# Performance work log

Measured on AMD Instinct MI355X. Metric: run time of the kernel, lower is better.

The kernel has to match this reference:

```python
import jax, jax.numpy as jnp
import numpy as np

N, D, K = 65536, 4096, 16
LN_EPS = 1e-5
SN_EPS = 1e-12
MIN_NORM = 1e-15


def setup_inputs() -> dict:
    key = jax.random.key(0)
    k1, k2, k3, k4 = jax.random.split(key, 4)
    return {
        "x": jax.random.normal(k1, (N, D), dtype=jnp.float32),
        "gamma": jnp.ones((D,), dtype=jnp.float32),
        "beta": jnp.zeros((D,), dtype=jnp.float32),
        "W": jax.random.normal(k2, (K, D), dtype=jnp.float32) * 0.02,
        "u": jax.random.normal(k3, (K,), dtype=jnp.float32),
        "log_scale": jnp.float32(-2.0),
    }


def _l2_normalize(v, eps=SN_EPS):
    return v / (jnp.linalg.norm(v) + eps)


def reference(x, gamma, beta, W, u, log_scale):
    # LayerNorm over last dim
    mean = jnp.mean(x, axis=-1, keepdims=True)
    var = jnp.mean(jnp.square(x - mean), axis=-1, keepdims=True)
    xn = (x - mean) * jax.lax.rsqrt(var + LN_EPS) * gamma + beta

    # spectral norm of W: one power iteration (torch spectral_norm forward)
    v = _l2_normalize(W.T @ u)           # [D]
    u_new = _l2_normalize(W @ v)         # [K]
    sigma = u_new @ (W @ v)              # scalar, top singular value estimate
    W_sn = W / sigma

    # linear (no bias) + learned scale
    vout = xn @ W_sn.T                   # [N, K]
    scale = jax.nn.sigmoid(log_scale) * 0.5
    vout = vout * scale

    # Poincare ball expmap0 with c=1: tanh(||v||) * v / ||v||
    vnorm = jnp.maximum(jnp.linalg.norm(vout, axis=-1, keepdims=True), MIN_NORM)
    return jnp.tanh(vnorm) * vout / vnorm
```

## Files before the change

### kernel.cpp

```cpp
#include <hip/hip_runtime.h>
#include <hip/hip_bf16.h>


#define ND 4096
#define NK 16
#define NROWS 65536

using f32x4  = __attribute__((ext_vector_type(4))) float;
using bf16x8 = __attribute__((ext_vector_type(8))) short;

#define GWB_OFF  0u
#define PART_OFF 131072u

__device__ __forceinline__ unsigned short f2bf(float f) {
    union { __hip_bfloat16 h; unsigned short u; } cv;
    cv.h = __float2bfloat16(f);
    return cv.u;
}

__global__ __launch_bounds__(256) void prep(
    const float* __restrict__ W, const float* __restrict__ gamma,
    const float* __restrict__ beta, const float* __restrict__ u,
    unsigned short* __restrict__ ws_gwb, float* __restrict__ ws_part)
{
    const int tid = threadIdx.x;
    const int d = blockIdx.x * 256 + tid;
    const int lane = tid & 63, wid = tid >> 6;

    float uu[NK];
#pragma unroll
    for (int k = 0; k < NK; ++k) uu[k] = u[k];
    const float g = gamma[d], b = beta[d];
    float w[NK];
#pragma unroll
    for (int k = 0; k < NK; ++k) w[k] = W[k * ND + d];

    float t = 0.f;
#pragma unroll
    for (int k = 0; k < NK; ++k) t = fmaf(w[k], uu[k], t);

    const int s  = d >> 5;
    const int wq = d & 31;
    const int lc = (wq >> 2) & 3;
    const int j  = (wq & 3) | ((wq >> 4) << 2);
    const int base = s * 512 + lc * 128 + j;

    float P[49];
#pragma unroll
    for (int k = 0; k < NK; ++k) {
        const float gw = g * w[k];
        ws_gwb[base + k * 8] = f2bf(gw);
        P[k]      = gw;
        P[16 + k] = b * w[k];
        P[32 + k] = w[k] * t;
    }
    P[48] = t * t;

#pragma unroll
    for (int m = 1; m < 64; m <<= 1) {
#pragma unroll
        for (int v = 0; v < 49; ++v) P[v] += __shfl_xor(P[v], m);
    }
    __shared__ float wred[4][49];
    if (lane == 0) {
#pragma unroll
        for (int v = 0; v < 49; ++v) wred[wid][v] = P[v];
    }
    __syncthreads();
    if (tid < 49)
        ws_part[blockIdx.x * 49 + tid] =
            (wred[0][tid] + wred[1][tid]) + (wred[2][tid] + wred[3][tid]);
}

__global__ __launch_bounds__(1024, 4) void hyp_main(
    const float* __restrict__ x, const unsigned short* __restrict__ gwb_g,
    const float* __restrict__ ws_part, const float* __restrict__ log_scale,
    float* __restrict__ out)
{
    __shared__ unsigned short gwb[ND * NK];
    __shared__ float scl[49];

    const int tid  = threadIdx.x;
    const int lane = tid & 63;
    const int wid  = tid >> 6;
    const int tile = (blockIdx.x << 4) + wid;
    const int lr = lane & 15;
    const int lc = lane >> 4;

    const float* xp = x + (size_t)(tile * 16 + lr) * ND + lc * 4;
    const unsigned short* lp = gwb + lane * 8;
    const int start = (tile * 53) & 63;

    const f32x4 xa0 = *(const f32x4*)(xp + start * 64);
    const f32x4 xb0 = *(const f32x4*)(xp + start * 64 + 16);
    const f32x4 xc0 = *(const f32x4*)(xp + start * 64 + 32);
    const f32x4 xd0 = *(const f32x4*)(xp + start * 64 + 48);

    {
        const uint4* src = (const uint4*)gwb_g;
        uint4* dst = (uint4*)gwb;
#pragma unroll
        for (int i = 0; i < 8; ++i)
            dst[tid + i * 1024] = src[tid + i * 1024];
    }
    if (tid < 49) {
        float s = 0.f;
#pragma unroll
        for (int b = 0; b < 16; ++b) s += ws_part[b * 49 + tid];
        scl[tid] = s;
    }
    __syncthreads();

    float ns2 = 0.f;
#pragma unroll
    for (int k = 0; k < NK; ++k) ns2 += scl[32 + k] * scl[32 + k];
    const float nt   = sqrtf(scl[48]) + 1e-12f;
    const float nwv  = sqrtf(ns2) / nt;
    const float sigma = (nwv * nwv) / (nwv + 1e-12f);
    const float coef = (0.5f / (1.0f + expf(-log_scale[0]))) / sigma;
    const float gk = scl[lr];
    const float bk = scl[16 + lr];

    f32x4 acc = {0.f, 0.f, 0.f, 0.f};
    float s1 = 0.f, s2 = 0.f;

#define HALF(XA, XB, SS) do {                                             \
        bf16x8 afrag;                                                     \
        afrag[0] = (short)f2bf(XA[0]); afrag[1] = (short)f2bf(XA[1]);     \
        afrag[2] = (short)f2bf(XA[2]); afrag[3] = (short)f2bf(XA[3]);     \
        afrag[4] = (short)f2bf(XB[0]); afrag[5] = (short)f2bf(XB[1]);     \
        afrag[6] = (short)f2bf(XB[2]); afrag[7] = (short)f2bf(XB[3]);     \
        s1 += ((XA[0] + XA[1]) + (XA[2] + XA[3]))                         \
            + ((XB[0] + XB[1]) + (XB[2] + XB[3]));                        \
        s2 = fmaf(XA[0], XA[0], s2); s2 = fmaf(XA[1], XA[1], s2);         \
        s2 = fmaf(XA[2], XA[2], s2); s2 = fmaf(XA[3], XA[3], s2);         \
        s2 = fmaf(XB[0], XB[0], s2); s2 = fmaf(XB[1], XB[1], s2);         \
        s2 = fmaf(XB[2], XB[2], s2); s2 = fmaf(XB[3], XB[3], s2);         \
        bf16x8 bfrag = *(const bf16x8*)(lp + (SS) * 512);                 \
        acc = __builtin_amdgcn_mfma_f32_16x16x32_bf16(afrag, bfrag, acc, 0, 0, 0); \
    } while (0)

#define PROCESS(II, XA, XB, XC, XD) do {                                  \
        HALF(XA, XB, 2 * (II));                                           \
        HALF(XC, XD, 2 * (II) + 1);                                       \
    } while (0)

#define LOADPROC(II) do {                                                 \
        f32x4 xa = *(const f32x4*)(xp + (II) * 64);                       \
        f32x4 xb = *(const f32x4*)(xp + (II) * 64 + 16);                  \
        f32x4 xc = *(const f32x4*)(xp + (II) * 64 + 32);                  \
        f32x4 xd = *(const f32x4*)(xp + (II) * 64 + 48);                  \
        PROCESS(II, xa, xb, xc, xd);                                      \
    } while (0)

    PROCESS(start, xa0, xb0, xc0, xd0);
#pragma unroll 2
    for (int i = start + 1; i < 64; ++i) LOADPROC(i);
#pragma unroll 2
    for (int i = 0; i < start; ++i) LOADPROC(i);
#undef LOADPROC
#undef PROCESS
#undef HALF

    s1 += __shfl_xor(s1, 16); s1 += __shfl_xor(s1, 32);
    s2 += __shfl_xor(s2, 16); s2 += __shfl_xor(s2, 32);
    const float mean = s1 * (1.0f / ND);
    const float var  = s2 * (1.0f / ND) - mean * mean;
    const float rstd = rsqrtf(var + 1e-5f);

    float vout[4];
#pragma unroll
    for (int j = 0; j < 4; ++j) {
        const int r = lc * 4 + j;
        const float m_r  = __shfl(mean, r);
        const float rs_r = __shfl(rstd, r);
        vout[j] = coef * (fmaf(-m_r, gk, acc[j]) * rs_r + bk);
    }

    float nsq[4];
#pragma unroll
    for (int j = 0; j < 4; ++j) nsq[j] = vout[j] * vout[j];
#pragma unroll
    for (int m = 1; m < 16; m <<= 1) {
#pragma unroll
        for (int j = 0; j < 4; ++j) nsq[j] += __shfl_xor(nsq[j], m);
    }

#pragma unroll
    for (int j = 0; j < 4; ++j) {
        float nv = sqrtf(nsq[j]);
        nv = fmaxf(nv, 1e-15f);
        const float fac = tanhf(nv) / nv;
        out[(size_t)(tile * 16 + lc * 4 + j) * NK + lr] = vout[j] * fac;
    }
}

extern "C" void kernel_launch(void* const* d_in, const int* in_sizes, int n_in,
                              void* d_out, int out_size, void* d_ws, size_t ws_size,
                              hipStream_t stream) {
    const float* x     = (const float*)d_in[0];
    const float* gamma = (const float*)d_in[1];
    const float* beta  = (const float*)d_in[2];
    const float* W     = (const float*)d_in[3];
    const float* u     = (const float*)d_in[4];
    const float* ls    = (const float*)d_in[5];

    char* ws = (char*)d_ws;
    unsigned short* ws_gwb = (unsigned short*)(ws + GWB_OFF);
    float* ws_part = (float*)(ws + PART_OFF);
    float* out     = (float*)d_out;

    prep<<<16, 256, 0, stream>>>(W, gamma, beta, u, ws_gwb, ws_part);
    hyp_main<<<256, 1024, 0, stream>>>(x, ws_gwb, ws_part, ls, out);
}
```

Measured before the change: 199.7 us.

## Fuse prep and main kernels into one cooperative launch with grid sync

Merges the small weight-prep kernel into the main kernel. The first 16 blocks compute the bf16 gamma*W table and the partial reductions, then every block waits on a cooperative grid-wide barrier before copying the table into LDS. The goal is to remove the second kernel launch and the gap between kernels, and to overlap the initial x prefetch with prep. In exchange it adds the cost of a grid barrier and requires all 256 blocks of 1024 threads to be co-resident, which the cooperative launch will reject if they are not.

```diff
diff --git a/kernel.cpp b/kernel.cpp
--- a/kernel.cpp
+++ b/kernel.cpp
@@ -1,5 +1,8 @@
 #include <hip/hip_runtime.h>
 #include <hip/hip_bf16.h>
+#include <hip/hip_cooperative_groups.h>
+
+namespace cg = cooperative_groups;
 
 
 #define ND 4096
@@ -18,66 +21,15 @@
     return cv.u;
 }
 
-__global__ __launch_bounds__(256) void prep(
-    const float* __restrict__ W, const float* __restrict__ gamma,
-    const float* __restrict__ beta, const float* __restrict__ u,
-    unsigned short* __restrict__ ws_gwb, float* __restrict__ ws_part)
-{
-    const int tid = threadIdx.x;
-    const int d = blockIdx.x * 256 + tid;
-    const int lane = tid & 63, wid = tid >> 6;
-
-    float uu[NK];
-#pragma unroll
-    for (int k = 0; k < NK; ++k) uu[k] = u[k];
-    const float g = gamma[d], b = beta[d];
-    float w[NK];
-#pragma unroll
-    for (int k = 0; k < NK; ++k) w[k] = W[k * ND + d];
-
-    float t = 0.f;
-#pragma unroll
-    for (int k = 0; k < NK; ++k) t = fmaf(w[k], uu[k], t);
-
-    const int s  = d >> 5;
-    const int wq = d & 31;
-    const int lc = (wq >> 2) & 3;
-    const int j  = (wq & 3) | ((wq >> 4) << 2);
-    const int base = s * 512 + lc * 128 + j;
-
-    float P[49];
-#pragma unroll
-    for (int k = 0; k < NK; ++k) {
-        const float gw = g * w[k];
-        ws_gwb[base + k * 8] = f2bf(gw);
-        P[k]      = gw;
-        P[16 + k] = b * w[k];
-        P[32 + k] = w[k] * t;
-    }
-    P[48] = t * t;
-
-#pragma unroll
-    for (int m = 1; m < 64; m <<= 1) {
-#pragma unroll
-        for (int v = 0; v < 49; ++v) P[v] += __shfl_xor(P[v], m);
-    }
-    __shared__ float wred[4][49];
-    if (lane == 0) {
-#pragma unroll
-        for (int v = 0; v < 49; ++v) wred[wid][v] = P[v];
-    }
-    __syncthreads();
-    if (tid < 49)
-        ws_part[blockIdx.x * 49 + tid] =
-            (wred[0][tid] + wred[1][tid]) + (wred[2][tid] + wred[3][tid]);
-}
-
-__global__ __launch_bounds__(1024, 4) void hyp_main(
-    const float* __restrict__ x, const unsigned short* __restrict__ gwb_g,
-    const float* __restrict__ ws_part, const float* __restrict__ log_scale,
+__global__ __launch_bounds__(1024, 4) void hyp_coop(
+    const float* __restrict__ x, const float* __restrict__ W,
+    const float* __restrict__ gamma, const float* __restrict__ beta,
+    const float* __restrict__ u, const float* __restrict__ log_scale,
+    unsigned short* __restrict__ ws_gwb, float* __restrict__ ws_part,
     float* __restrict__ out)
 {
     __shared__ unsigned short gwb[ND * NK];
+    __shared__ float wred[4][49];
     __shared__ float scl[49];
 
     const int tid  = threadIdx.x;
@@ -96,8 +48,57 @@
     const f32x4 xc0 = *(const f32x4*)(xp + start * 64 + 32);
     const f32x4 xd0 = *(const f32x4*)(xp + start * 64 + 48);
 
+    if (blockIdx.x < 16 && tid < 256) {
+        const int d = blockIdx.x * 256 + tid;
+        float uu[NK];
+#pragma unroll
+        for (int k = 0; k < NK; ++k) uu[k] = u[k];
+        const float g = gamma[d], b = beta[d];
+        float w[NK];
+#pragma unroll
+        for (int k = 0; k < NK; ++k) w[k] = W[k * ND + d];
+
+        float t = 0.f;
+#pragma unroll
+        for (int k = 0; k < NK; ++k) t = fmaf(w[k], uu[k], t);
+
+        const int s_  = d >> 5;
+        const int wq  = d & 31;
+        const int lcw = (wq >> 2) & 3;
+        const int jw  = (wq & 3) | ((wq >> 4) << 2);
+        const int base = s_ * 512 + lcw * 128 + jw;
+
+        float P[49];
+#pragma unroll
+        for (int k = 0; k < NK; ++k) {
+            const float gw = g * w[k];
+            ws_gwb[base + k * 8] = f2bf(gw);
+            P[k]      = gw;
+            P[16 + k] = b * w[k];
+            P[32 + k] = w[k] * t;
+        }
+        P[48] = t * t;
+
+#pragma unroll
+        for (int m = 1; m < 64; m <<= 1) {
+#pragma unroll
+            for (int v = 0; v < 49; ++v) P[v] += __shfl_xor(P[v], m);
+        }
+        if (lane == 0) {
+#pragma unroll
+            for (int v = 0; v < 49; ++v) wred[tid >> 6][v] = P[v];
+        }
+    }
+    __syncthreads();
+    if (blockIdx.x < 16 && tid < 49)
+        ws_part[blockIdx.x * 49 + tid] =
+            (wred[0][tid] + wred[1][tid]) + (wred[2][tid] + wred[3][tid]);
+
+    __threadfence();
+    cg::this_grid().sync();
+
     {
-        const uint4* src = (const uint4*)gwb_g;
+        const uint4* src = (const uint4*)ws_gwb;
         uint4* dst = (uint4*)gwb;
 #pragma unroll
         for (int i = 0; i < 8; ++i)
@@ -210,6 +211,10 @@
     float* ws_part = (float*)(ws + PART_OFF);
     float* out     = (float*)d_out;
 
-    prep<<<16, 256, 0, stream>>>(W, gamma, beta, u, ws_gwb, ws_part);
-    hyp_main<<<256, 1024, 0, stream>>>(x, ws_gwb, ws_part, ls, out);
+    void* args[] = {
+        (void*)&x, (void*)&W, (void*)&gamma, (void*)&beta, (void*)&u,
+        (void*)&ls, (void*)&ws_gwb, (void*)&ws_part, (void*)&out
+    };
+    hipLaunchCooperativeKernel((const void*)hyp_coop, dim3(256), dim3(1024),
+                               args, 0, stream);
 }
```

Result: slower. 299.5 us (+50.0%).

## Read bf16 weight fragments from global memory instead of staging in LDS

Applied to the files above, without the earlier changes.

Drops the 128KB LDS staging of the gamma-scaled bf16 weight matrix and has each wave load its B fragments directly from global memory (served from L2/L1), and shrinks blocks to 256 threads with 1024 blocks. This removes the per-block LDS copy and barrier wait before compute, and lifts the LDS occupancy limit so more waves can hide HBM latency on the streaming x reads. In exchange, every wave fetches weight fragments through the cache hierarchy, which adds cache traffic alongside the x stream. The loop is also restructured to process one 32-column step per iteration with a rotated start offset.

```diff
diff --git a/kernel.cpp b/kernel.cpp
--- a/kernel.cpp
+++ b/kernel.cpp
@@ -72,37 +72,28 @@
             (wred[0][tid] + wred[1][tid]) + (wred[2][tid] + wred[3][tid]);
 }
 
-__global__ __launch_bounds__(1024, 4) void hyp_main(
+__global__ __launch_bounds__(256, 8) void hyp_main(
     const float* __restrict__ x, const unsigned short* __restrict__ gwb_g,
     const float* __restrict__ ws_part, const float* __restrict__ log_scale,
     float* __restrict__ out)
 {
-    __shared__ unsigned short gwb[ND * NK];
     __shared__ float scl[49];
 
     const int tid  = threadIdx.x;
     const int lane = tid & 63;
     const int wid  = tid >> 6;
-    const int tile = (blockIdx.x << 4) + wid;
+    const int tile = (blockIdx.x << 2) + wid;
     const int lr = lane & 15;
     const int lc = lane >> 4;
 
     const float* xp = x + (size_t)(tile * 16 + lr) * ND + lc * 4;
-    const unsigned short* lp = gwb + lane * 8;
-    const int start = (tile * 53) & 63;
+    const unsigned short* bp = gwb_g + lane * 8;
+    const int start = (tile * 53) & 127;
 
-    const f32x4 xa0 = *(const f32x4*)(xp + start * 64);
-    const f32x4 xb0 = *(const f32x4*)(xp + start * 64 + 16);
-    const f32x4 xc0 = *(const f32x4*)(xp + start * 64 + 32);
-    const f32x4 xd0 = *(const f32x4*)(xp + start * 64 + 48);
+    const f32x4 xa0 = *(const f32x4*)(xp + start * 32);
+    const f32x4 xb0 = *(const f32x4*)(xp + start * 32 + 16);
+    const bf16x8 bf0 = *(const bf16x8*)(bp + start * 512);
 
-    {
-        const uint4* src = (const uint4*)gwb_g;
-        uint4* dst = (uint4*)gwb;
-#pragma unroll
-        for (int i = 0; i < 8; ++i)
-            dst[tid + i * 1024] = src[tid + i * 1024];
-    }
     if (tid < 49) {
         float s = 0.f;
 #pragma unroll
@@ -124,7 +115,7 @@
     f32x4 acc = {0.f, 0.f, 0.f, 0.f};
     float s1 = 0.f, s2 = 0.f;
 
-#define HALF(XA, XB, SS) do {                                             \
+#define PROC_BODY(XA, XB, BF) do {                                        \
         bf16x8 afrag;                                                     \
         afrag[0] = (short)f2bf(XA[0]); afrag[1] = (short)f2bf(XA[1]);     \
         afrag[2] = (short)f2bf(XA[2]); afrag[3] = (short)f2bf(XA[3]);     \
@@ -136,31 +127,23 @@
         s2 = fmaf(XA[2], XA[2], s2); s2 = fmaf(XA[3], XA[3], s2);         \
         s2 = fmaf(XB[0], XB[0], s2); s2 = fmaf(XB[1], XB[1], s2);         \
         s2 = fmaf(XB[2], XB[2], s2); s2 = fmaf(XB[3], XB[3], s2);         \
-        bf16x8 bfrag = *(const bf16x8*)(lp + (SS) * 512);                 \
-        acc = __builtin_amdgcn_mfma_f32_16x16x32_bf16(afrag, bfrag, acc, 0, 0, 0); \
+        acc = __builtin_amdgcn_mfma_f32_16x16x32_bf16(afrag, (BF), acc, 0, 0, 0); \
     } while (0)
 
-#define PROCESS(II, XA, XB, XC, XD) do {                                  \
-        HALF(XA, XB, 2 * (II));                                           \
-        HALF(XC, XD, 2 * (II) + 1);                                       \
+#define PROCESS(SS) do {                                                  \
+        f32x4 xa = *(const f32x4*)(xp + (SS) * 32);                       \
+        f32x4 xb = *(const f32x4*)(xp + (SS) * 32 + 16);                  \
+        bf16x8 bfr = *(const bf16x8*)(bp + (SS) * 512);                   \
+        PROC_BODY(xa, xb, bfr);                                           \
     } while (0)
 
-#define LOADPROC(II) do {                                                 \
-        f32x4 xa = *(const f32x4*)(xp + (II) * 64);                       \
-        f32x4 xb = *(const f32x4*)(xp + (II) * 64 + 16);                  \
-        f32x4 xc = *(const f32x4*)(xp + (II) * 64 + 32);                  \
-        f32x4 xd = *(const f32x4*)(xp + (II) * 64 + 48);                  \
-        PROCESS(II, xa, xb, xc, xd);                                      \
-    } while (0)
-
-    PROCESS(start, xa0, xb0, xc0, xd0);
+    PROC_BODY(xa0, xb0, bf0);
 #pragma unroll 2
-    for (int i = start + 1; i < 64; ++i) LOADPROC(i);
+    for (int s = start + 1; s < 128; ++s) PROCESS(s);
 #pragma unroll 2
-    for (int i = 0; i < start; ++i) LOADPROC(i);
-#undef LOADPROC
+    for (int s = 0; s < start; ++s) PROCESS(s);
 #undef PROCESS
-#undef HALF
+#undef PROC_BODY
 
     s1 += __shfl_xor(s1, 16); s1 += __shfl_xor(s1, 32);
     s2 += __shfl_xor(s2, 16); s2 += __shfl_xor(s2, 32);
@@ -211,5 +194,5 @@
     float* out     = (float*)d_out;
 
     prep<<<16, 256, 0, stream>>>(W, gamma, beta, u, ws_gwb, ws_part);
-    hyp_main<<<256, 1024, 0, stream>>>(x, ws_gwb, ws_part, ls, out);
+    hyp_main<<<1024, 256, 0, stream>>>(x, ws_gwb, ws_part, ls, out);
 }
```

Measured after the change: 188.2 us (median of 2 runs). 5.8% less time.
